# Kernel tuning notes

Hardware: AMD Instinct MI355X
Metric: run time of the kernel (lower is better)

Reference implementation:

```python
import jax, jax.numpy as jnp
import numpy as np

B, C, N = 64, 81, 8732
SCALE_XY, SCALE_WH = 10.0, 5.0  # inverses of dboxes.scale_xy=0.1, scale_wh=0.2


def setup_inputs() -> dict:
    key = jax.random.key(0)
    k1, k2, k3, k4, k5 = jax.random.split(key, 5)
    ploc = jax.random.normal(k1, (B, 4, N), dtype=jnp.float32)
    plabel = jax.random.normal(k2, (B, C, N), dtype=jnp.float32)
    # gloc wh must be positive (log of ratio); keep xy positive too (box coords)
    gloc = jax.random.uniform(k3, (B, 4, N), dtype=jnp.float32, minval=0.05, maxval=1.0)
    glabel = jax.random.randint(k4, (B, N), 0, C).astype(jnp.int64)
    # default boxes in xywh, wh strictly positive
    dboxes = jax.random.uniform(k5, (1, 4, N), dtype=jnp.float32, minval=0.05, maxval=1.0)
    return {"ploc": ploc, "plabel": plabel, "gloc": gloc, "glabel": glabel, "dboxes": dboxes}


def reference(ploc, plabel, gloc, glabel, dboxes):
    f32 = ploc.dtype
    mask = glabel > 0                                   # [B,N] positives
    pos_num = mask.sum(axis=1)                          # [B]

    # _location_vec: encode ground-truth boxes relative to default boxes
    gxy = SCALE_XY * (gloc[:, :2, :] - dboxes[:, :2, :]) / dboxes[:, 2:, :]
    gwh = SCALE_WH * jnp.log(gloc[:, 2:, :] / dboxes[:, 2:, :])
    vec_gd = jnp.concatenate([gxy, gwh], axis=1)        # [B,4,N]

    # smooth-L1 per element, summed over the 4 coord channels
    d = ploc - vec_gd
    ad = jnp.abs(d)
    sl1 = jnp.where(ad < 1.0, 0.5 * d * d, ad - 0.5)
    loc_loss = (mask.astype(f32) * sl1.sum(axis=1)).sum(axis=1)  # [B]

    # per-anchor cross entropy: -log_softmax over class dim gathered at glabel
    logp = jax.nn.log_softmax(plabel, axis=1)           # [B,C,N]
    con = -jnp.take_along_axis(logp, glabel[:, None, :], axis=1)[:, 0, :]  # [B,N]

    # hard negative mining: rank negatives by CE descending, keep top 3*pos_num
    con_neg = jnp.where(mask, 0.0, con)
    idx = jnp.argsort(-con_neg, axis=1)                 # descending sort indices
    rank = jnp.argsort(idx, axis=1)                     # rank of each anchor
    neg_num = jnp.minimum(3 * pos_num, N)[:, None]      # [B,1]
    neg_mask = rank < neg_num                           # [B,N]

    con_loss = (con * (mask.astype(f32) + neg_mask.astype(f32))).sum(axis=1)  # [B]

    total_loss = loc_loss + con_loss
    num_mask = (pos_num > 0).astype(f32)
    posf = jnp.clip(pos_num.astype(f32), 1e-6)
    return (total_loss * num_mask / posf).mean()
```

## Files before the change

### kernel.cpp

```cpp
#include <hip/hip_runtime.h>
#include <math.h>

#define BATCH 64
#define NCLS 81
#define NANCH 8732
#define NQ (NANCH / 4)
#define K1_CHUNKS ((NQ + 255) / 256)

#define LOG2E 1.44269504088896340736f
#define LN2   0.69314718055994530942f

__global__ __launch_bounds__(256) void k1_con_loc(
    const float* __restrict__ ploc, const float* __restrict__ plabel,
    const float* __restrict__ gloc, const int* __restrict__ glabel,
    const float* __restrict__ dboxes, float* __restrict__ con_out,
    float* __restrict__ loc_acc, float* __restrict__ conpos_acc,
    float* __restrict__ consum_acc, int* __restrict__ pos_acc)
{
    const int b = blockIdx.x / K1_CHUNKS;
    const int q = (blockIdx.x % K1_CHUNKS) * 256 + threadIdx.x;

    float locsum = 0.f, conpos = 0.f, consum = 0.f;
    int poscnt = 0;

    if (q < NQ) {
        const int n = q * 4;
        int4 labv = *(const int4*)(glabel + (size_t)b * NANCH + n);
        int lab[4] = {labv.x, labv.y, labv.z, labv.w};

        float s[4] = {0.f, 0.f, 0.f, 0.f};
        float xl[4] = {0.f, 0.f, 0.f, 0.f};

        const float* pb = plabel + (size_t)b * NCLS * NANCH + n;
        for (int c = 0; c < NCLS; ++c) {
            float4 xv = *(const float4*)(pb + (size_t)c * NANCH);
            float x[4] = {xv.x, xv.y, xv.z, xv.w};
            #pragma unroll
            for (int a = 0; a < 4; ++a) {
                s[a] += __builtin_amdgcn_exp2f(x[a] * LOG2E);
                if (c == lab[a]) xl[a] = x[a];
            }
        }
        float con[4];
        #pragma unroll
        for (int a = 0; a < 4; ++a) {
            con[a] = LN2 * __builtin_amdgcn_logf(s[a]) - xl[a];
            consum += con[a];
        }
        *(float4*)(con_out + (size_t)b * NANCH + n) =
            make_float4(con[0], con[1], con[2], con[3]);

        union F4 { float4 v; float f[4]; };
        F4 p[4], g[4], d[4];
        const float* pl = ploc + (size_t)b * 4 * NANCH + n;
        const float* gl = gloc + (size_t)b * 4 * NANCH + n;
        const float* db = dboxes + n;
        #pragma unroll
        for (int ch = 0; ch < 4; ++ch) {
            p[ch].v = *(const float4*)(pl + (size_t)ch * NANCH);
            g[ch].v = *(const float4*)(gl + (size_t)ch * NANCH);
            d[ch].v = *(const float4*)(db + (size_t)ch * NANCH);
        }
        #pragma unroll
        for (int a = 0; a < 4; ++a) {
            float vg0 = 10.f * (g[0].f[a] - d[0].f[a]) / d[2].f[a];
            float vg1 = 10.f * (g[1].f[a] - d[1].f[a]) / d[3].f[a];
            float vg2 = 5.f * LN2 * __builtin_amdgcn_logf(g[2].f[a] / d[2].f[a]);
            float vg3 = 5.f * LN2 * __builtin_amdgcn_logf(g[3].f[a] / d[3].f[a]);
            float d0 = p[0].f[a] - vg0, d1 = p[1].f[a] - vg1;
            float d2 = p[2].f[a] - vg2, d3 = p[3].f[a] - vg3;
            float sl = 0.f, ad;
            ad = fabsf(d0); sl += (ad < 1.f) ? 0.5f * d0 * d0 : ad - 0.5f;
            ad = fabsf(d1); sl += (ad < 1.f) ? 0.5f * d1 * d1 : ad - 0.5f;
            ad = fabsf(d2); sl += (ad < 1.f) ? 0.5f * d2 * d2 : ad - 0.5f;
            ad = fabsf(d3); sl += (ad < 1.f) ? 0.5f * d3 * d3 : ad - 0.5f;
            if (lab[a] > 0) { locsum += sl; conpos += con[a]; poscnt += 1; }
        }
    }

    for (int o = 32; o; o >>= 1) {
        locsum += __shfl_down(locsum, o, 64);
        conpos += __shfl_down(conpos, o, 64);
        consum += __shfl_down(consum, o, 64);
        poscnt += __shfl_down(poscnt, o, 64);
    }
    __shared__ float rl[4], rc[4], rs[4];
    __shared__ int rp[4];
    int lane = threadIdx.x & 63, wid = threadIdx.x >> 6;
    if (lane == 0) { rl[wid] = locsum; rc[wid] = conpos; rs[wid] = consum; rp[wid] = poscnt; }
    __syncthreads();
    if (threadIdx.x == 0) {
        float L = 0.f, Cp = 0.f, Cs = 0.f; int P = 0;
        for (int w = 0; w < 4; ++w) { L += rl[w]; Cp += rc[w]; Cs += rs[w]; P += rp[w]; }
        atomicAdd(loc_acc + b, L);
        atomicAdd(conpos_acc + b, Cp);
        atomicAdd(consum_acc + b, Cs);
        atomicAdd(pos_acc + b, P);
    }
}

__global__ __launch_bounds__(1024) void k2_mine(
    const float* __restrict__ con, const int* __restrict__ glabel,
    const float* __restrict__ loc_acc, const float* __restrict__ conpos_acc,
    const float* __restrict__ consum_acc, const int* __restrict__ pos_acc,
    float* __restrict__ batch_loss)
{
    const int b = blockIdx.x;
    const int tid = threadIdx.x;
    const int lane = tid & 63, wid = tid >> 6;

    const int pos = pos_acc[b];
    int Ki = 3 * pos; if (Ki > NANCH) Ki = NANCH;

    if (3 * pos >= NANCH) {
        if (tid == 0) {
            float total = loc_acc[b] + conpos_acc[b] + consum_acc[b];
            float posf = fmaxf((float)pos, 1e-6f);
            batch_loss[b] = total / posf;
        }
        return;
    }

    __shared__ unsigned int bits[NANCH];
    __shared__ unsigned int hist[256];
    __shared__ unsigned int sh_t, sh_cnt;
    __shared__ unsigned int wtots[16];
    __shared__ float wsum[16];

    const float* cb = con + (size_t)b * NANCH;
    const int* lb = glabel + (size_t)b * NANCH;

    for (int i = tid; i < NANCH; i += 1024) {
        float c = cb[i];
        int l = lb[i];
        bits[i] = (l > 0) ? 0u : __float_as_uint(fmaxf(c, 0.f));
    }
    __syncthreads();

    float sel = 0.f;
    if (Ki > 0) {
        unsigned int rem = (unsigned)Ki, hi = 0u;
        for (int shift = 24; shift >= 0; shift -= 8) {
            for (int i = tid; i < 256; i += 1024) hist[i] = 0u;
            __syncthreads();
            for (int i = tid; i < NANCH; i += 1024) {
                unsigned v = bits[i];
                unsigned up = (shift == 24) ? 0u : (v >> (shift + 8));
                if (up == hi) atomicAdd(&hist[(v >> shift) & 255u], 1u);
            }
            __syncthreads();
            if (tid == 0) {
                unsigned cum = 0;
                for (int t = 255; t >= 0; --t) {
                    unsigned h = hist[t];
                    if (cum + h >= rem) { sh_t = (unsigned)t; sh_cnt = cum; break; }
                    cum += h;
                }
            }
            __syncthreads();
            hi = (hi << 8) | sh_t;
            rem -= sh_cnt;
            __syncthreads();
        }
        const unsigned T = hi;
        const unsigned need = rem;

        float local = 0.f;
        for (int i = tid; i < NANCH; i += 1024)
            if (bits[i] > T) local += cb[i];

        unsigned running = 0;
        for (int base = 0; base < NANCH; base += 1024) {
            int i = base + tid;
            bool flag = (i < NANCH) && (bits[i] == T);
            unsigned long long bal = __ballot(flag);
            int lr = __popcll(bal & ((1ULL << lane) - 1ULL));
            int wt = __popcll(bal);
            if (lane == 0) wtots[wid] = (unsigned)wt;
            __syncthreads();
            unsigned woff = 0, btot = 0;
            for (int w = 0; w < 16; ++w) { if (w < wid) woff += wtots[w]; btot += wtots[w]; }
            if (flag && (running + woff + (unsigned)lr) < need) local += cb[i];
            running += btot;
            __syncthreads();
        }

        for (int o = 32; o; o >>= 1) local += __shfl_down(local, o, 64);
        if (lane == 0) wsum[wid] = local;
        __syncthreads();
        if (tid == 0) { for (int w = 0; w < 16; ++w) sel += wsum[w]; }
    }

    if (tid == 0) {
        float total = loc_acc[b] + conpos_acc[b] + sel;
        float numm = (pos > 0) ? 1.f : 0.f;
        float posf = fmaxf((float)pos, 1e-6f);
        batch_loss[b] = total * numm / posf;
    }
}

__global__ void k3_mean(const float* __restrict__ batch_loss, float* __restrict__ out)
{
    float v = batch_loss[threadIdx.x];
    for (int o = 32; o; o >>= 1) v += __shfl_down(v, o, 64);
    if (threadIdx.x == 0) out[0] = v / (float)BATCH;
}

extern "C" void kernel_launch(void* const* d_in, const int* in_sizes, int n_in,
                              void* d_out, int out_size, void* d_ws, size_t ws_size,
                              hipStream_t stream)
{
    const float* ploc   = (const float*)d_in[0];
    const float* plabel = (const float*)d_in[1];
    const float* gloc   = (const float*)d_in[2];
    const int*   glabel = (const int*)d_in[3];
    const float* dboxes = (const float*)d_in[4];

    float* con        = (float*)d_ws;
    float* loc_acc    = con + (size_t)BATCH * NANCH;
    float* conpos_acc = loc_acc + BATCH;
    float* consum_acc = conpos_acc + BATCH;
    int*   pos_acc    = (int*)(consum_acc + BATCH);
    float* batch_loss = (float*)(pos_acc + BATCH);

    (void)hipMemsetAsync(loc_acc, 0, 4 * BATCH * sizeof(float), stream);

    k1_con_loc<<<BATCH * K1_CHUNKS, 256, 0, stream>>>(
        ploc, plabel, gloc, glabel, dboxes, con, loc_acc, conpos_acc, consum_acc, pos_acc);
    k2_mine<<<BATCH, 1024, 0, stream>>>(
        con, glabel, loc_acc, conpos_acc, consum_acc, pos_acc, batch_loss);
    k3_mean<<<1, 64, 0, stream>>>(batch_loss, (float*)d_out);
}
```

Baseline: 276.7 us.

## Split class-dimension sum-exp across three blocks with partial buffers

```diff
diff --git a/kernel.cpp b/kernel.cpp
--- a/kernel.cpp
+++ b/kernel.cpp
@@ -6,16 +6,55 @@
 #define NANCH 8732
 #define NQ (NANCH / 4)
 #define K1_CHUNKS ((NQ + 255) / 256)
+#define SPLIT 3
+#define CPS (NCLS / SPLIT)
 
 #define LOG2E 1.44269504088896340736f
 #define LN2   0.69314718055994530942f
 
-__global__ __launch_bounds__(256) void k1_con_loc(
-    const float* __restrict__ ploc, const float* __restrict__ plabel,
-    const float* __restrict__ gloc, const int* __restrict__ glabel,
-    const float* __restrict__ dboxes, float* __restrict__ con_out,
-    float* __restrict__ loc_acc, float* __restrict__ conpos_acc,
-    float* __restrict__ consum_acc, int* __restrict__ pos_acc)
+union F4 { float4 v; float f[4]; };
+
+__global__ __launch_bounds__(256) void k1a_sumexp(
+    const float* __restrict__ plabel, const int* __restrict__ glabel,
+    float* __restrict__ spart, float* __restrict__ xlpart)
+{
+    const int split = blockIdx.x / (BATCH * K1_CHUNKS);
+    const int rest  = blockIdx.x % (BATCH * K1_CHUNKS);
+    const int b     = rest / K1_CHUNKS;
+    const int q     = (rest % K1_CHUNKS) * 256 + threadIdx.x;
+    if (q >= NQ) return;
+    const int n = q * 4;
+
+    int4 labv = *(const int4*)(glabel + (size_t)b * NANCH + n);
+    int lab[4] = {labv.x, labv.y, labv.z, labv.w};
+
+    const int c0 = split * CPS;
+    float s[4]  = {0.f, 0.f, 0.f, 0.f};
+    float xl[4] = {0.f, 0.f, 0.f, 0.f};
+
+    const float* pb = plabel + (size_t)b * NCLS * NANCH + (size_t)c0 * NANCH + n;
+    #pragma unroll 9
+    for (int c = 0; c < CPS; ++c) {
+        float4 xv = *(const float4*)(pb + (size_t)c * NANCH);
+        float x[4] = {xv.x, xv.y, xv.z, xv.w};
+        #pragma unroll
+        for (int a = 0; a < 4; ++a) {
+            s[a] += __builtin_amdgcn_exp2f(x[a] * LOG2E);
+            if (c0 + c == lab[a]) xl[a] = x[a];
+        }
+    }
+    const size_t o = ((size_t)split * BATCH + b) * NANCH + n;
+    *(float4*)(spart + o)  = make_float4(s[0], s[1], s[2], s[3]);
+    *(float4*)(xlpart + o) = make_float4(xl[0], xl[1], xl[2], xl[3]);
+}
+
+__global__ __launch_bounds__(256) void k1b_finalize(
+    const float* __restrict__ ploc, const float* __restrict__ gloc,
+    const int* __restrict__ glabel, const float* __restrict__ dboxes,
+    const float* __restrict__ spart, const float* __restrict__ xlpart,
+    float* __restrict__ con_out, float* __restrict__ loc_acc,
+    float* __restrict__ conpos_acc, float* __restrict__ consum_acc,
+    int* __restrict__ pos_acc)
 {
     const int b = blockIdx.x / K1_CHUNKS;
     const int q = (blockIdx.x % K1_CHUNKS) * 256 + threadIdx.x;
@@ -28,29 +67,25 @@
         int4 labv = *(const int4*)(glabel + (size_t)b * NANCH + n);
         int lab[4] = {labv.x, labv.y, labv.z, labv.w};
 
-        float s[4] = {0.f, 0.f, 0.f, 0.f};
-        float xl[4] = {0.f, 0.f, 0.f, 0.f};
-
-        const float* pb = plabel + (size_t)b * NCLS * NANCH + n;
-        for (int c = 0; c < NCLS; ++c) {
-            float4 xv = *(const float4*)(pb + (size_t)c * NANCH);
-            float x[4] = {xv.x, xv.y, xv.z, xv.w};
-            #pragma unroll
-            for (int a = 0; a < 4; ++a) {
-                s[a] += __builtin_amdgcn_exp2f(x[a] * LOG2E);
-                if (c == lab[a]) xl[a] = x[a];
-            }
-        }
+        F4 sp[SPLIT], xp[SPLIT];
+        #pragma unroll
+        for (int k = 0; k < SPLIT; ++k) {
+            const size_t o = ((size_t)k * BATCH + b) * NANCH + n;
+            sp[k].v = *(const float4*)(spart + o);
+            xp[k].v = *(const float4*)(xlpart + o);
+        }
+
         float con[4];
         #pragma unroll
         for (int a = 0; a < 4; ++a) {
-            con[a] = LN2 * __builtin_amdgcn_logf(s[a]) - xl[a];
+            float s  = sp[0].f[a] + sp[1].f[a] + sp[2].f[a];
+            float xl = xp[0].f[a] + xp[1].f[a] + xp[2].f[a];
+            con[a] = LN2 * __builtin_amdgcn_logf(s) - xl;
             consum += con[a];
         }
         *(float4*)(con_out + (size_t)b * NANCH + n) =
             make_float4(con[0], con[1], con[2], con[3]);
 
-        union F4 { float4 v; float f[4]; };
         F4 p[4], g[4], d[4];
         const float* pl = ploc + (size_t)b * 4 * NANCH + n;
         const float* gl = gloc + (size_t)b * 4 * NANCH + n;
@@ -217,7 +252,9 @@
     const float* dboxes = (const float*)d_in[4];
 
     float* con        = (float*)d_ws;
-    float* loc_acc    = con + (size_t)BATCH * NANCH;
+    float* spart      = con + (size_t)BATCH * NANCH;
+    float* xlpart     = spart + (size_t)SPLIT * BATCH * NANCH;
+    float* loc_acc    = xlpart + (size_t)SPLIT * BATCH * NANCH;
     float* conpos_acc = loc_acc + BATCH;
     float* consum_acc = conpos_acc + BATCH;
     int*   pos_acc    = (int*)(consum_acc + BATCH);
@@ -225,8 +262,11 @@
 
     (void)hipMemsetAsync(loc_acc, 0, 4 * BATCH * sizeof(float), stream);
 
-    k1_con_loc<<<BATCH * K1_CHUNKS, 256, 0, stream>>>(
-        ploc, plabel, gloc, glabel, dboxes, con, loc_acc, conpos_acc, consum_acc, pos_acc);
+    k1a_sumexp<<<BATCH * K1_CHUNKS * SPLIT, 256, 0, stream>>>(
+        plabel, glabel, spart, xlpart);
+    k1b_finalize<<<BATCH * K1_CHUNKS, 256, 0, stream>>>(
+        ploc, gloc, glabel, dboxes, spart, xlpart,
+        con, loc_acc, conpos_acc, consum_acc, pos_acc);
     k2_mine<<<BATCH, 1024, 0, stream>>>(
         con, glabel, loc_acc, conpos_acc, consum_acc, pos_acc, batch_loss);
     k3_mean<<<1, 64, 0, stream>>>(batch_loss, (float*)d_out);
```

Measured after the change: 287.4 us. 3.9% more time.

## Map one anchor per thread, batch class loads, and replace atomics with per-block partials

Applied to the files above, without the earlier changes.

```diff
diff --git a/kernel.cpp b/kernel.cpp
--- a/kernel.cpp
+++ b/kernel.cpp
@@ -4,8 +4,8 @@
 #define BATCH 64
 #define NCLS 81
 #define NANCH 8732
-#define NQ (NANCH / 4)
-#define K1_CHUNKS ((NQ + 255) / 256)
+#define NCHUNK 35
+#define CBATCH 16
 
 #define LOG2E 1.44269504088896340736f
 #define LN2   0.69314718055994530942f
@@ -14,69 +14,63 @@
     const float* __restrict__ ploc, const float* __restrict__ plabel,
     const float* __restrict__ gloc, const int* __restrict__ glabel,
     const float* __restrict__ dboxes, float* __restrict__ con_out,
-    float* __restrict__ loc_acc, float* __restrict__ conpos_acc,
-    float* __restrict__ consum_acc, int* __restrict__ pos_acc)
-{
-    const int b = blockIdx.x / K1_CHUNKS;
-    const int q = (blockIdx.x % K1_CHUNKS) * 256 + threadIdx.x;
-
-    float locsum = 0.f, conpos = 0.f, consum = 0.f;
-    int poscnt = 0;
-
-    if (q < NQ) {
-        const int n = q * 4;
-        int4 labv = *(const int4*)(glabel + (size_t)b * NANCH + n);
-        int lab[4] = {labv.x, labv.y, labv.z, labv.w};
-
-        float s[4] = {0.f, 0.f, 0.f, 0.f};
-        float xl[4] = {0.f, 0.f, 0.f, 0.f};
-
-        const float* pb = plabel + (size_t)b * NCLS * NANCH + n;
-        for (int c = 0; c < NCLS; ++c) {
-            float4 xv = *(const float4*)(pb + (size_t)c * NANCH);
-            float x[4] = {xv.x, xv.y, xv.z, xv.w};
-            #pragma unroll
-            for (int a = 0; a < 4; ++a) {
-                s[a] += __builtin_amdgcn_exp2f(x[a] * LOG2E);
-                if (c == lab[a]) xl[a] = x[a];
-            }
-        }
-        float con[4];
+    float* __restrict__ loc_part, float* __restrict__ conpos_part,
+    float* __restrict__ consum_part, int* __restrict__ pos_part)
+{
+    const int b     = blockIdx.x / NCHUNK;
+    const int chunk = blockIdx.x % NCHUNK;
+    const int nn    = chunk * 256 + threadIdx.x;
+    const bool act  = nn < NANCH;
+    const int nc    = act ? nn : (NANCH - 1);
+
+    const int lab = glabel[(size_t)b * NANCH + nc];
+
+    float s = 0.f, xl = 0.f;
+    const float* pb = plabel + (size_t)b * NCLS * NANCH + nc;
+    #pragma unroll 1
+    for (int cc = 0; cc < NCLS - 1; cc += CBATCH) {
+        float xv[CBATCH];
         #pragma unroll
-        for (int a = 0; a < 4; ++a) {
-            con[a] = LN2 * __builtin_amdgcn_logf(s[a]) - xl[a];
-            consum += con[a];
-        }
-        *(float4*)(con_out + (size_t)b * NANCH + n) =
-            make_float4(con[0], con[1], con[2], con[3]);
-
-        union F4 { float4 v; float f[4]; };
-        F4 p[4], g[4], d[4];
-        const float* pl = ploc + (size_t)b * 4 * NANCH + n;
-        const float* gl = gloc + (size_t)b * 4 * NANCH + n;
-        const float* db = dboxes + n;
+        for (int j = 0; j < CBATCH; ++j)
+            xv[j] = pb[(size_t)(cc + j) * NANCH];
         #pragma unroll
-        for (int ch = 0; ch < 4; ++ch) {
-            p[ch].v = *(const float4*)(pl + (size_t)ch * NANCH);
-            g[ch].v = *(const float4*)(gl + (size_t)ch * NANCH);
-            d[ch].v = *(const float4*)(db + (size_t)ch * NANCH);
-        }
-        #pragma unroll
-        for (int a = 0; a < 4; ++a) {
-            float vg0 = 10.f * (g[0].f[a] - d[0].f[a]) / d[2].f[a];
-            float vg1 = 10.f * (g[1].f[a] - d[1].f[a]) / d[3].f[a];
-            float vg2 = 5.f * LN2 * __builtin_amdgcn_logf(g[2].f[a] / d[2].f[a]);
-            float vg3 = 5.f * LN2 * __builtin_amdgcn_logf(g[3].f[a] / d[3].f[a]);
-            float d0 = p[0].f[a] - vg0, d1 = p[1].f[a] - vg1;
-            float d2 = p[2].f[a] - vg2, d3 = p[3].f[a] - vg3;
-            float sl = 0.f, ad;
-            ad = fabsf(d0); sl += (ad < 1.f) ? 0.5f * d0 * d0 : ad - 0.5f;
-            ad = fabsf(d1); sl += (ad < 1.f) ? 0.5f * d1 * d1 : ad - 0.5f;
-            ad = fabsf(d2); sl += (ad < 1.f) ? 0.5f * d2 * d2 : ad - 0.5f;
-            ad = fabsf(d3); sl += (ad < 1.f) ? 0.5f * d3 * d3 : ad - 0.5f;
-            if (lab[a] > 0) { locsum += sl; conpos += con[a]; poscnt += 1; }
-        }
-    }
+        for (int j = 0; j < CBATCH; ++j) {
+            s += __builtin_amdgcn_exp2f(xv[j] * LOG2E);
+            if (cc + j == lab) xl = xv[j];
+        }
+    }
+    {
+        float xv = pb[(size_t)(NCLS - 1) * NANCH];
+        s += __builtin_amdgcn_exp2f(xv * LOG2E);
+        if (NCLS - 1 == lab) xl = xv;
+    }
+
+    const float con = LN2 * __builtin_amdgcn_logf(s) - xl;
+    if (act) con_out[(size_t)b * NANCH + nn] = con;
+
+    const float* pl = ploc + (size_t)b * 4 * NANCH + nc;
+    const float* gl = gloc + (size_t)b * 4 * NANCH + nc;
+    const float* db = dboxes + nc;
+    float p0 = pl[0], p1 = pl[NANCH], p2 = pl[2 * NANCH], p3 = pl[3 * NANCH];
+    float g0 = gl[0], g1 = gl[NANCH], g2 = gl[2 * NANCH], g3 = gl[3 * NANCH];
+    float d0v = db[0], d1v = db[NANCH], d2v = db[2 * NANCH], d3v = db[3 * NANCH];
+
+    float vg0 = 10.f * (g0 - d0v) / d2v;
+    float vg1 = 10.f * (g1 - d1v) / d3v;
+    float vg2 = 5.f * LN2 * __builtin_amdgcn_logf(g2 / d2v);
+    float vg3 = 5.f * LN2 * __builtin_amdgcn_logf(g3 / d3v);
+    float e0 = p0 - vg0, e1 = p1 - vg1, e2 = p2 - vg2, e3 = p3 - vg3;
+    float sl = 0.f, ad;
+    ad = fabsf(e0); sl += (ad < 1.f) ? 0.5f * e0 * e0 : ad - 0.5f;
+    ad = fabsf(e1); sl += (ad < 1.f) ? 0.5f * e1 * e1 : ad - 0.5f;
+    ad = fabsf(e2); sl += (ad < 1.f) ? 0.5f * e2 * e2 : ad - 0.5f;
+    ad = fabsf(e3); sl += (ad < 1.f) ? 0.5f * e3 * e3 : ad - 0.5f;
+
+    const bool ispos = act && (lab > 0);
+    float locsum = ispos ? sl : 0.f;
+    float conpos = ispos ? con : 0.f;
+    float consum = act ? con : 0.f;
+    int poscnt = ispos ? 1 : 0;
 
     for (int o = 32; o; o >>= 1) {
         locsum += __shfl_down(locsum, o, 64);
@@ -92,31 +86,51 @@
     if (threadIdx.x == 0) {
         float L = 0.f, Cp = 0.f, Cs = 0.f; int P = 0;
         for (int w = 0; w < 4; ++w) { L += rl[w]; Cp += rc[w]; Cs += rs[w]; P += rp[w]; }
-        atomicAdd(loc_acc + b, L);
-        atomicAdd(conpos_acc + b, Cp);
-        atomicAdd(consum_acc + b, Cs);
-        atomicAdd(pos_acc + b, P);
+        loc_part[blockIdx.x] = L;
+        conpos_part[blockIdx.x] = Cp;
+        consum_part[blockIdx.x] = Cs;
+        pos_part[blockIdx.x] = P;
     }
 }
 
 __global__ __launch_bounds__(1024) void k2_mine(
     const float* __restrict__ con, const int* __restrict__ glabel,
-    const float* __restrict__ loc_acc, const float* __restrict__ conpos_acc,
-    const float* __restrict__ consum_acc, const int* __restrict__ pos_acc,
+    const float* __restrict__ loc_part, const float* __restrict__ conpos_part,
+    const float* __restrict__ consum_part, const int* __restrict__ pos_part,
     float* __restrict__ batch_loss)
 {
     const int b = blockIdx.x;
     const int tid = threadIdx.x;
     const int lane = tid & 63, wid = tid >> 6;
 
-    const int pos = pos_acc[b];
+    __shared__ float sh_loccon, sh_tot;
+    __shared__ int sh_pos;
+    {
+        float lv = 0.f, cv = 0.f, sv = 0.f; int pv = 0;
+        if (tid < NCHUNK) {
+            lv = loc_part[b * NCHUNK + tid];
+            cv = conpos_part[b * NCHUNK + tid];
+            sv = consum_part[b * NCHUNK + tid];
+            pv = pos_part[b * NCHUNK + tid];
+        }
+        if (tid < 64) {
+            for (int o = 32; o; o >>= 1) {
+                lv += __shfl_down(lv, o, 64);
+                cv += __shfl_down(cv, o, 64);
+                sv += __shfl_down(sv, o, 64);
+                pv += __shfl_down(pv, o, 64);
+            }
+            if (tid == 0) { sh_loccon = lv + cv; sh_tot = lv + cv + sv; sh_pos = pv; }
+        }
+    }
+    __syncthreads();
+    const int pos = sh_pos;
     int Ki = 3 * pos; if (Ki > NANCH) Ki = NANCH;
 
     if (3 * pos >= NANCH) {
         if (tid == 0) {
-            float total = loc_acc[b] + conpos_acc[b] + consum_acc[b];
             float posf = fmaxf((float)pos, 1e-6f);
-            batch_loss[b] = total / posf;
+            batch_loss[b] = sh_tot / posf;
         }
         return;
     }
@@ -192,7 +206,7 @@
     }
 
     if (tid == 0) {
-        float total = loc_acc[b] + conpos_acc[b] + sel;
+        float total = sh_loccon + sel;
         float numm = (pos > 0) ? 1.f : 0.f;
         float posf = fmaxf((float)pos, 1e-6f);
         batch_loss[b] = total * numm / posf;
@@ -216,18 +230,17 @@
     const int*   glabel = (const int*)d_in[3];
     const float* dboxes = (const float*)d_in[4];
 
-    float* con        = (float*)d_ws;
-    float* loc_acc    = con + (size_t)BATCH * NANCH;
-    float* conpos_acc = loc_acc + BATCH;
-    float* consum_acc = conpos_acc + BATCH;
-    int*   pos_acc    = (int*)(consum_acc + BATCH);
-    float* batch_loss = (float*)(pos_acc + BATCH);
-
-    (void)hipMemsetAsync(loc_acc, 0, 4 * BATCH * sizeof(float), stream);
-
-    k1_con_loc<<<BATCH * K1_CHUNKS, 256, 0, stream>>>(
-        ploc, plabel, gloc, glabel, dboxes, con, loc_acc, conpos_acc, consum_acc, pos_acc);
+    float* con         = (float*)d_ws;
+    float* loc_part    = con + (size_t)BATCH * NANCH;
+    float* conpos_part = loc_part + BATCH * NCHUNK;
+    float* consum_part = conpos_part + BATCH * NCHUNK;
+    int*   pos_part    = (int*)(consum_part + BATCH * NCHUNK);
+    float* batch_loss  = (float*)(pos_part + BATCH * NCHUNK);
+
+    k1_con_loc<<<BATCH * NCHUNK, 256, 0, stream>>>(
+        ploc, plabel, gloc, glabel, dboxes, con,
+        loc_part, conpos_part, consum_part, pos_part);
     k2_mine<<<BATCH, 1024, 0, stream>>>(
-        con, glabel, loc_acc, conpos_acc, consum_acc, pos_acc, batch_loss);
+        con, glabel, loc_part, conpos_part, consum_part, pos_part, batch_loss);
     k3_mean<<<1, 64, 0, stream>>>(batch_loss, (float*)d_out);
 }
```

Result: no change. 274.8 us (-0.7%).
